# Optimization experiments

Hardware: AMD Instinct MI355X
Metric: run time of the kernel (lower is better)

Reference implementation:

```python
import jax, jax.numpy as jnp
import numpy as np

N, C, H, W, K = 8, 32, 512, 512, 6   # batch, embed dim, image HW, max components per image
MIN_PIX = 20
EPS = 1e-6
MARGIN = 0.5
L_INTER, L_INST, L_BG, L_SCENE = 0.4, 0.1, 0.2, 0.5


def _build_labels():
    # K disjoint 'subtitle line' rectangles per image; label 0 = background.
    # This is exactly what cv2.connectedComponents would return on the gt mask.
    labels = np.zeros((N, H, W), np.int32)
    for n in range(N):
        for k in range(K):
            r0 = 30 + k * 75
            c0 = 60 + (n % 3) * 20
            labels[n, r0:r0 + 40, c0:c0 + 300] = k + 1
    return labels


def setup_inputs() -> dict:
    key = jax.random.key(0)
    k1, k2 = jax.random.split(key)
    labels = _build_labels()
    gt = (labels > 0).astype(np.float32)[:, None]          # [N,1,H,W]
    color = jax.random.normal(k1, (N, C, H, W), jnp.float32)
    binary = jax.random.uniform(k2, (N, 1, H, W), jnp.float32)  # pred binary map
    return {"color": color, "gt": jnp.asarray(gt), "binary": binary,
            "comp_labels": jnp.asarray(labels)}


def _safe_norm(d2):
    # torch.norm = sqrt(sum sq); tiny floor avoids NaN grads at exactly 0
    return jnp.sqrt(jnp.maximum(d2, 1e-12))


def reference(color, gt, binary, comp_labels):
    f32 = color.dtype
    sub = (gt[:, 0] > 0.5).astype(f32)                                   # [N,H,W]
    text = (jax.lax.stop_gradient(binary)[:, 0] > 0.5).astype(f32)       # detached
    scene = text * (1.0 - sub)
    bg = (1.0 - sub) * (1.0 - scene)

    # one-hot component masks [N,K,H,W]
    comp = (comp_labels[:, None, :, :] ==
            jnp.arange(1, K + 1, dtype=comp_labels.dtype)[None, :, None, None]).astype(f32)
    cnt = comp.sum((2, 3))                                               # [N,K]

    # per-component first/second moments via batched segment-reduce
    S1 = jnp.einsum('nchw,nkhw->nkc', color, comp)                       # sum of feat
    fsq = (color * color).sum(1)                                         # [N,H,W]
    S2 = jnp.einsum('nhw,nkhw->nk', fsq, comp)                           # sum of |feat|^2
    m_inst = S1 / (cnt + EPS)[:, :, None]                                # [N,K,C]
    # sum over comp pixels of |f - m|^2, divided by (cnt+eps)
    intra_k = (S2 - 2.0 * (m_inst * S1).sum(-1)
               + cnt * (m_inst * m_inst).sum(-1)) / (cnt + EPS)

    sub_cnt = sub.sum((1, 2)); bg_cnt = bg.sum((1, 2)); scene_cnt = scene.sum((1, 2))
    m_sub = jnp.einsum('nchw,nhw->nc', color, sub) / (sub_cnt + EPS)[:, None]
    m_bg = jnp.einsum('nchw,nhw->nc', color, bg) / (bg_cnt + EPS)[:, None]
    m_scene = jnp.einsum('nchw,nhw->nc', color, scene) / (scene_cnt + EPS)[:, None]

    comp_big = cnt >= MIN_PIX                                            # [N,K]
    n_valid = comp_big.sum(1)                                            # [N]
    item_valid = (bg_cnt >= MIN_PIX) & (n_valid >= 1)
    cv = comp_big & item_valid[:, None]
    total = cv.sum()

    intra_sum = jnp.where(cv, intra_k, 0.0).sum()

    d_inst_bg = _safe_norm(((m_inst - m_bg[:, None, :]) ** 2).sum(-1))   # [N,K]
    inter_sum = jnp.where(cv, jax.nn.relu(MARGIN - d_inst_bg) ** 2, 0.0).sum()

    item_multi = item_valid & (n_valid > 1)
    d2_inst_sub = ((m_inst - m_sub[:, None, :]) ** 2).sum(-1)
    inst_sum = jnp.where(cv & item_multi[:, None], d2_inst_sub, 0.0).sum()
    inst_n = jnp.where(item_multi, n_valid, 0).sum()

    bg_cond = item_valid & (sub_cnt >= MIN_PIX)
    d_sub_bg = _safe_norm(((m_sub - m_bg) ** 2).sum(-1))
    subbg_sum = jnp.where(bg_cond, jax.nn.relu(MARGIN - d_sub_bg) ** 2, 0.0).sum()
    subbg_n = bg_cond.sum()

    sc_cond = item_valid & (scene_cnt >= MIN_PIX) & (sub_cnt >= MIN_PIX)
    d_sub_sc = _safe_norm(((m_sub - m_scene) ** 2).sum(-1))
    subsc_sum = jnp.where(sc_cond, jax.nn.relu(2.0 * MARGIN - d_sub_sc) ** 2, 0.0).sum()
    subsc_n = sc_cond.sum()

    def avg(s, n):
        return jnp.where(n > 0, s / jnp.maximum(n, 1).astype(f32), 0.0)

    loss = (avg(intra_sum, total)
            + L_INTER * avg(inter_sum, total)
            + L_INST * avg(inst_sum, inst_n)
            + L_BG * avg(subbg_sum, subbg_n)
            + L_SCENE * avg(subsc_sum, subsc_n))
    return jnp.where(total > 0, loss, jnp.zeros((), f32))
```

## Files before the change

kernel.cpp:

```cpp
#include <hip/hip_runtime.h>


#define NIMG   8
#define NCH    32
#define IMHW   (512 * 512)
#define STRIPE 1024
#define BPI    (IMHW / STRIPE)
#define WSN    304

__device__ __forceinline__ float redhalf(float x) {
    x += __shfl_xor(x, 1);
    x += __shfl_xor(x, 2);
    x += __shfl_xor(x, 4);
    x += __shfl_xor(x, 8);
    x += __shfl_xor(x, 16);
    return x;
}

__device__ __forceinline__ float red64(float x) {
    x += __shfl_xor(x, 1);
    x += __shfl_xor(x, 2);
    x += __shfl_xor(x, 4);
    x += __shfl_xor(x, 8);
    x += __shfl_xor(x, 16);
    x += __shfl_xor(x, 32);
    return x;
}

__device__ __forceinline__ void comp_pass(
    const float* __restrict__ colc, int pix0,
    const unsigned* __restrict__ codes, int l32, int c, int L2, float* lds)
{
    float aL = 0.f, s2 = 0.f;
#pragma unroll
    for (int j = 0; j < STRIPE; j += 128) {
        const int off = j + (l32 << 2);
        const float4 v4 = *reinterpret_cast<const float4*>(colc + pix0 + off);
        const unsigned cw = codes[off >> 2];
        const float vv[4] = {v4.x, v4.y, v4.z, v4.w};
#pragma unroll
        for (int e = 0; e < 4; ++e) {
            const int l = (int)((cw >> (8 * e + 2)) & 0x3Fu);
            const float mv = (l == L2) ? vv[e] : 0.f;
            aL += mv;
            s2 = fmaf(mv, mv, s2);
        }
    }
    aL = redhalf(aL); s2 = redhalf(s2);
    if (l32 == 0 && L2 >= 1 && L2 <= 6) {
        atomicAdd(&lds[96 + (L2 - 1) * 32 + c], aL);
        atomicAdd(&lds[297 + (L2 - 1)], s2);
    }
}

__global__ __launch_bounds__(256, 8) void scl_main(
    const float* __restrict__ color, const float* __restrict__ gt,
    const float* __restrict__ bin, const int* __restrict__ lab,
    float* __restrict__ ws)
{
    __shared__ float lds[WSN];
    __shared__ unsigned codes[STRIPE / 4];
    __shared__ int labmask;

    const int tid = threadIdx.x;
    for (int i = tid; i < WSN; i += 256) lds[i] = 0.f;
    if (tid == 0) labmask = 0;

    const int n    = blockIdx.x / BPI;
    const int pix0 = (blockIdx.x % BPI) * STRIPE;

    const float* gtn  = gt  + (size_t)n * IMHW;
    const float* binn = bin + (size_t)n * IMHW;
    const int*   labn = lab + (size_t)n * IMHW;
    const float* coln = color + (size_t)n * NCH * IMHW;

    const int off1 = tid << 2;
    {
        const int p = pix0 + off1;
        const float4 g4 = *reinterpret_cast<const float4*>(gtn + p);
        const float4 b4 = *reinterpret_cast<const float4*>(binn + p);
        const int4   l4 = *reinterpret_cast<const int4*>(labn + p);
        const float gg[4] = {g4.x, g4.y, g4.z, g4.w};
        const float bb[4] = {b4.x, b4.y, b4.z, b4.w};
        const int   ll[4] = {l4.x, l4.y, l4.z, l4.w};
        unsigned wrd = 0; int lm = 0;
        float c0 = 0.f, c1 = 0.f;
        float ck[6] = {0.f, 0.f, 0.f, 0.f, 0.f, 0.f};
#pragma unroll
        for (int e = 0; e < 4; ++e) {
            const bool sub  = gg[e] > 0.5f;
            const bool text = bb[e] > 0.5f;
            const int  r    = sub ? 0 : (text ? 1 : 2);
            const int  l    = ll[e];
            wrd |= (unsigned)((l << 2) | r) << (8 * e);
            lm  |= 1 << l;
            c0  += (r == 0) ? 1.f : 0.f;
            c1  += (r == 1) ? 1.f : 0.f;
#pragma unroll
            for (int kk = 0; kk < 6; ++kk)
                ck[kk] += (l == kk + 1) ? 1.f : 0.f;
        }
        codes[tid] = wrd;
        __syncthreads();

        c0 = red64(c0); c1 = red64(c1);
#pragma unroll
        for (int kk = 0; kk < 6; ++kk) ck[kk] = red64(ck[kk]);
        lm |= __shfl_xor(lm, 1);  lm |= __shfl_xor(lm, 2);
        lm |= __shfl_xor(lm, 4);  lm |= __shfl_xor(lm, 8);
        lm |= __shfl_xor(lm, 16); lm |= __shfl_xor(lm, 32);
        if ((tid & 63) == 0) {
            atomicAdd(&lds[288], c0);
            atomicAdd(&lds[289], c1);
#pragma unroll
            for (int kk = 0; kk < 6; ++kk) atomicAdd(&lds[291 + kk], ck[kk]);
            atomicOr(&labmask, lm);
        }
    }
    __syncthreads();

    const unsigned cmask = ((unsigned)labmask) & ~1u;
    const int Lc = cmask ? (__ffs(cmask) - 1) : 255;

    const int lane = tid & 63;
    const int wv   = tid >> 6;
    const int half = lane >> 5;
    const int l32  = lane & 31;

    for (int cpi = 0; cpi < 4; ++cpi) {
        const int cp = wv * 4 + cpi;
        const int c  = cp * 2 + half;
        const float* colc = coln + (size_t)c * IMHW;

        float vt = 0.f, s0 = 0.f, s1 = 0.f, aL = 0.f, s2 = 0.f;
#pragma unroll
        for (int j = 0; j < STRIPE; j += 128) {
            const int off = j + (l32 << 2);
            const float4 v4 = *reinterpret_cast<const float4*>(colc + pix0 + off);
            const unsigned cw = codes[off >> 2];
            const float vv[4] = {v4.x, v4.y, v4.z, v4.w};
#pragma unroll
            for (int e = 0; e < 4; ++e) {
                const float v = vv[e];
                const int r = (int)((cw >> (8 * e)) & 3u);
                const int l = (int)((cw >> (8 * e + 2)) & 0x3Fu);
                vt += v;
                s0 += (r == 0) ? v : 0.f;
                s1 += (r == 1) ? v : 0.f;
                const float mv = (l == Lc) ? v : 0.f;
                aL += mv;
                s2 = fmaf(mv, mv, s2);
            }
        }

        vt = redhalf(vt); s0 = redhalf(s0); s1 = redhalf(s1);
        aL = redhalf(aL); s2 = redhalf(s2);

        if (l32 == 0) {
            atomicAdd(&lds[ 0 + c], s0);
            atomicAdd(&lds[32 + c], s1);
            atomicAdd(&lds[64 + c], vt);
            if (Lc <= 6) {
                atomicAdd(&lds[96 + (Lc - 1) * 32 + c], aL);
                atomicAdd(&lds[297 + (Lc - 1)], s2);
            }
        }
    }

    unsigned extra = cmask ? (cmask & (cmask - 1)) : 0u;
    while (extra) {
        const int L2 = __ffs(extra) - 1; extra &= extra - 1;
        for (int cpi = 0; cpi < 4; ++cpi) {
            const int cp = wv * 4 + cpi;
            const int c  = cp * 2 + half;
            comp_pass(coln + (size_t)c * IMHW, pix0, codes, l32, c, L2, lds);
        }
    }
    __syncthreads();

    float* wsn = ws + (size_t)n * WSN;
    for (int i = tid; i < WSN; i += 256) {
        const float v = lds[i];
        if (v != 0.f) atomicAdd(&wsn[i], v);
    }
}

__global__ void scl_final(const float* __restrict__ ws, float* __restrict__ out)
{
    const int lane = threadIdx.x;
    const int n = lane / 6;
    const int k = lane - n * 6;
    const bool active = lane < 48;

    float t_cv = 0.f, t_intra = 0.f, t_inter = 0.f, t_inst = 0.f, t_instn = 0.f;
    float t_sbg = 0.f, t_sbgn = 0.f, t_ssc = 0.f, t_sscn = 0.f;

    if (active) {
        const float* w = ws + (size_t)n * WSN;
        const float cnt    = w[291 + k];
        const float s2     = w[297 + k];
        const float subc   = w[288];
        const float scenec = w[289];
        const float bgc    = 262144.f - subc - scenec;

        float nv = 0.f;
#pragma unroll
        for (int kk = 0; kk < 6; ++kk) nv += (w[291 + kk] >= 20.f) ? 1.f : 0.f;

        const bool comp_big   = cnt >= 20.f;
        const bool item_valid = (bgc >= 20.f) && (nv >= 1.f);
        const bool cv         = comp_big && item_valid;

        const float den  = cnt + 1e-6f;
        const float dsub = subc + 1e-6f;
        const float dbg  = bgc + 1e-6f;
        const float dsc  = scenec + 1e-6f;

        float dot_mS1 = 0.f, dot_mm = 0.f, d2bg = 0.f, d2sub = 0.f;
        for (int c = 0; c < 32; ++c) {
            const float S1 = w[96 + k * 32 + c];
            const float m  = S1 / den;
            dot_mS1 = fmaf(m, S1, dot_mS1);
            dot_mm  = fmaf(m, m, dot_mm);
            const float msub = w[c] / dsub;
            const float mbg  = (w[64 + c] - w[c] - w[32 + c]) / dbg;
            float d = m - mbg;  d2bg  = fmaf(d, d, d2bg);
            d = m - msub;       d2sub = fmaf(d, d, d2sub);
        }
        const float intra_k = (s2 - 2.f * dot_mS1 + cnt * dot_mm) / den;

        if (cv) {
            t_cv = 1.f;
            t_intra = intra_k;
            const float dd = sqrtf(fmaxf(d2bg, 1e-12f));
            const float r  = fmaxf(0.5f - dd, 0.f);
            t_inter = r * r;
        }
        const bool multi = item_valid && (nv > 1.f);
        if (cv && multi) t_inst = d2sub;

        if (k == 0) {
            if (multi) t_instn = nv;
            const bool bgcond = item_valid && (subc >= 20.f);
            const bool sccond = item_valid && (scenec >= 20.f) && (subc >= 20.f);
            float d2sb = 0.f, d2ss = 0.f;
            for (int c = 0; c < 32; ++c) {
                const float msub = w[c] / dsub;
                const float mbg  = (w[64 + c] - w[c] - w[32 + c]) / dbg;
                const float msc  = w[32 + c] / dsc;
                float a = msub - mbg; d2sb = fmaf(a, a, d2sb);
                float b = msub - msc; d2ss = fmaf(b, b, d2ss);
            }
            if (bgcond) {
                const float dd = sqrtf(fmaxf(d2sb, 1e-12f));
                const float r  = fmaxf(0.5f - dd, 0.f);
                t_sbg = r * r; t_sbgn = 1.f;
            }
            if (sccond) {
                const float dd = sqrtf(fmaxf(d2ss, 1e-12f));
                const float r  = fmaxf(1.0f - dd, 0.f);
                t_ssc = r * r; t_sscn = 1.f;
            }
        }
    }

#define RED64(x) { x += __shfl_xor(x, 1); x += __shfl_xor(x, 2); x += __shfl_xor(x, 4); \
                   x += __shfl_xor(x, 8); x += __shfl_xor(x, 16); x += __shfl_xor(x, 32); }
    RED64(t_cv) RED64(t_intra) RED64(t_inter) RED64(t_inst) RED64(t_instn)
    RED64(t_sbg) RED64(t_sbgn) RED64(t_ssc) RED64(t_sscn)
#undef RED64

    if (lane == 0) {
        const float total = t_cv;
        auto avg = [](float s, float nn) { return nn > 0.f ? s / fmaxf(nn, 1.f) : 0.f; };
        const float loss = avg(t_intra, total)
                         + 0.4f * avg(t_inter, total)
                         + 0.1f * avg(t_inst, t_instn)
                         + 0.2f * avg(t_sbg, t_sbgn)
                         + 0.5f * avg(t_ssc, t_sscn);
        out[0] = (total > 0.f) ? loss : 0.f;
    }
}

extern "C" void kernel_launch(void* const* d_in, const int* in_sizes, int n_in,
                              void* d_out, int out_size, void* d_ws, size_t ws_size,
                              hipStream_t stream)
{
    (void)in_sizes; (void)n_in; (void)out_size; (void)ws_size;
    const float* color = (const float*)d_in[0];
    const float* gt    = (const float*)d_in[1];
    const float* bin   = (const float*)d_in[2];
    const int*   lab   = (const int*)d_in[3];
    float* ws  = (float*)d_ws;
    float* out = (float*)d_out;

    hipMemsetAsync(ws, 0, (size_t)NIMG * WSN * sizeof(float), stream);
    hipLaunchKernelGGL(scl_main, dim3(NIMG * BPI), dim3(256), 0, stream,
                       color, gt, bin, lab, ws);
    hipLaunchKernelGGL(scl_final, dim3(1), dim3(64), 0, stream, ws, out);
}
```

Measured before the change: 404.8 us.

## Split mask coding into separate kernel and spread channels across four blocks

Moves the per-pixel mask/label coding into its own kernel that writes packed codes and per-chunk label masks to workspace. The color pass then launches four blocks per chunk, each handling 8 channels, which gives more parallelism and less serial work per block. Blocks now accumulate directly into global memory with atomics rather than through shared memory. The cost is an extra launch, a round trip for the codes through global memory, and more global atomic traffic.

```diff
diff --git a/kernel.cpp b/kernel.cpp
--- a/kernel.cpp
+++ b/kernel.cpp
@@ -4,184 +4,179 @@
 #define NIMG   8
 #define NCH    32
 #define IMHW   (512 * 512)
-#define STRIPE 1024
-#define BPI    (IMHW / STRIPE)
+#define CHUNK  1024
+#define CPI    (IMHW / CHUNK)
 #define WSN    304
+#define LC_OFF    12288
+#define CODES_OFF 16384
 
 __device__ __forceinline__ float redhalf(float x) {
-    x += __shfl_xor(x, 1);
-    x += __shfl_xor(x, 2);
-    x += __shfl_xor(x, 4);
-    x += __shfl_xor(x, 8);
-    x += __shfl_xor(x, 16);
+    x += __shfl_xor(x, 1);  x += __shfl_xor(x, 2);  x += __shfl_xor(x, 4);
+    x += __shfl_xor(x, 8);  x += __shfl_xor(x, 16);
     return x;
 }
-
 __device__ __forceinline__ float red64(float x) {
-    x += __shfl_xor(x, 1);
-    x += __shfl_xor(x, 2);
-    x += __shfl_xor(x, 4);
-    x += __shfl_xor(x, 8);
-    x += __shfl_xor(x, 16);
-    x += __shfl_xor(x, 32);
-    return x;
-}
-
-__device__ __forceinline__ void comp_pass(
-    const float* __restrict__ colc, int pix0,
-    const unsigned* __restrict__ codes, int l32, int c, int L2, float* lds)
+    x = redhalf(x); x += __shfl_xor(x, 32); return x;
+}
+
+__global__ __launch_bounds__(256) void scl_codes(
+    const float* __restrict__ gt, const float* __restrict__ bin,
+    const int* __restrict__ lab, float* __restrict__ ws,
+    unsigned char* __restrict__ lc, unsigned* __restrict__ codes)
 {
-    float aL = 0.f, s2 = 0.f;
-#pragma unroll
-    for (int j = 0; j < STRIPE; j += 128) {
-        const int off = j + (l32 << 2);
-        const float4 v4 = *reinterpret_cast<const float4*>(colc + pix0 + off);
-        const unsigned cw = codes[off >> 2];
-        const float vv[4] = {v4.x, v4.y, v4.z, v4.w};
-#pragma unroll
-        for (int e = 0; e < 4; ++e) {
-            const int l = (int)((cw >> (8 * e + 2)) & 0x3Fu);
-            const float mv = (l == L2) ? vv[e] : 0.f;
-            aL += mv;
-            s2 = fmaf(mv, mv, s2);
-        }
-    }
-    aL = redhalf(aL); s2 = redhalf(s2);
-    if (l32 == 0 && L2 >= 1 && L2 <= 6) {
-        atomicAdd(&lds[96 + (L2 - 1) * 32 + c], aL);
-        atomicAdd(&lds[297 + (L2 - 1)], s2);
-    }
-}
-
-__global__ __launch_bounds__(256, 8) void scl_main(
-    const float* __restrict__ color, const float* __restrict__ gt,
-    const float* __restrict__ bin, const int* __restrict__ lab,
+    __shared__ float ldsc[8];
+    __shared__ int labmask;
+    const int tid = threadIdx.x;
+    if (tid < 8) ldsc[tid] = 0.f;
+    if (tid == 0) labmask = 0;
+
+    const int n = blockIdx.x / CPI;
+    const int q = blockIdx.x % CPI;
+    const int base = n * IMHW + q * CHUNK;
+    const int p = base + (tid << 2);
+
+    const float4 g4 = *reinterpret_cast<const float4*>(gt + p);
+    const float4 b4 = *reinterpret_cast<const float4*>(bin + p);
+    const int4   l4 = *reinterpret_cast<const int4*>(lab + p);
+    const float gg[4] = {g4.x, g4.y, g4.z, g4.w};
+    const float bb[4] = {b4.x, b4.y, b4.z, b4.w};
+    const int   ll[4] = {l4.x, l4.y, l4.z, l4.w};
+
+    unsigned wrd = 0; int lm = 0;
+    float c0 = 0.f, c1 = 0.f;
+    float ck[6] = {0.f, 0.f, 0.f, 0.f, 0.f, 0.f};
+#pragma unroll
+    for (int e = 0; e < 4; ++e) {
+        const bool sub  = gg[e] > 0.5f;
+        const bool text = bb[e] > 0.5f;
+        const int  r    = sub ? 0 : (text ? 1 : 2);
+        unsigned   ul   = (unsigned)ll[e];
+        if (ul > 7u) ul = 7u;
+        wrd |= ((ul << 2) | (unsigned)r) << (8 * e);
+        lm  |= 1 << ul;
+        c0  += (r == 0) ? 1.f : 0.f;
+        c1  += (r == 1) ? 1.f : 0.f;
+#pragma unroll
+        for (int kk = 0; kk < 6; ++kk)
+            ck[kk] += (ul == (unsigned)(kk + 1)) ? 1.f : 0.f;
+    }
+    codes[(base >> 2) + tid] = wrd;
+
+    c0 = red64(c0); c1 = red64(c1);
+#pragma unroll
+    for (int kk = 0; kk < 6; ++kk) ck[kk] = red64(ck[kk]);
+    lm |= __shfl_xor(lm, 1);  lm |= __shfl_xor(lm, 2);  lm |= __shfl_xor(lm, 4);
+    lm |= __shfl_xor(lm, 8);  lm |= __shfl_xor(lm, 16); lm |= __shfl_xor(lm, 32);
+
+    __syncthreads();
+    if ((tid & 63) == 0) {
+        atomicAdd(&ldsc[0], c0);
+        atomicAdd(&ldsc[1], c1);
+#pragma unroll
+        for (int kk = 0; kk < 6; ++kk) atomicAdd(&ldsc[2 + kk], ck[kk]);
+        atomicOr(&labmask, lm);
+    }
+    __syncthreads();
+
+    float* wsn = ws + (size_t)n * WSN;
+    if (tid == 0) {
+        lc[n * CPI + q] = (unsigned char)((labmask >> 1) & 0x3F);
+        atomicAdd(&wsn[288], ldsc[0]);
+        atomicAdd(&wsn[289], ldsc[1]);
+    }
+    if (tid >= 2 && tid < 8) atomicAdd(&wsn[291 + (tid - 2)], ldsc[tid]);
+}
+
+__global__ __launch_bounds__(256) void scl_color(
+    const float* __restrict__ color, const float* __restrict__ ws_ro,
+    const unsigned char* __restrict__ lc, const unsigned* __restrict__ codes,
     float* __restrict__ ws)
 {
-    __shared__ float lds[WSN];
-    __shared__ unsigned codes[STRIPE / 4];
-    __shared__ int labmask;
-
-    const int tid = threadIdx.x;
-    for (int i = tid; i < WSN; i += 256) lds[i] = 0.f;
-    if (tid == 0) labmask = 0;
-
-    const int n    = blockIdx.x / BPI;
-    const int pix0 = (blockIdx.x % BPI) * STRIPE;
-
-    const float* gtn  = gt  + (size_t)n * IMHW;
-    const float* binn = bin + (size_t)n * IMHW;
-    const int*   labn = lab + (size_t)n * IMHW;
-    const float* coln = color + (size_t)n * NCH * IMHW;
-
-    const int off1 = tid << 2;
-    {
-        const int p = pix0 + off1;
-        const float4 g4 = *reinterpret_cast<const float4*>(gtn + p);
-        const float4 b4 = *reinterpret_cast<const float4*>(binn + p);
-        const int4   l4 = *reinterpret_cast<const int4*>(labn + p);
-        const float gg[4] = {g4.x, g4.y, g4.z, g4.w};
-        const float bb[4] = {b4.x, b4.y, b4.z, b4.w};
-        const int   ll[4] = {l4.x, l4.y, l4.z, l4.w};
-        unsigned wrd = 0; int lm = 0;
-        float c0 = 0.f, c1 = 0.f;
-        float ck[6] = {0.f, 0.f, 0.f, 0.f, 0.f, 0.f};
-#pragma unroll
-        for (int e = 0; e < 4; ++e) {
-            const bool sub  = gg[e] > 0.5f;
-            const bool text = bb[e] > 0.5f;
-            const int  r    = sub ? 0 : (text ? 1 : 2);
-            const int  l    = ll[e];
-            wrd |= (unsigned)((l << 2) | r) << (8 * e);
-            lm  |= 1 << l;
-            c0  += (r == 0) ? 1.f : 0.f;
-            c1  += (r == 1) ? 1.f : 0.f;
-#pragma unroll
-            for (int kk = 0; kk < 6; ++kk)
-                ck[kk] += (l == kk + 1) ? 1.f : 0.f;
-        }
-        codes[tid] = wrd;
-        __syncthreads();
-
-        c0 = red64(c0); c1 = red64(c1);
-#pragma unroll
-        for (int kk = 0; kk < 6; ++kk) ck[kk] = red64(ck[kk]);
-        lm |= __shfl_xor(lm, 1);  lm |= __shfl_xor(lm, 2);
-        lm |= __shfl_xor(lm, 4);  lm |= __shfl_xor(lm, 8);
-        lm |= __shfl_xor(lm, 16); lm |= __shfl_xor(lm, 32);
-        if ((tid & 63) == 0) {
-            atomicAdd(&lds[288], c0);
-            atomicAdd(&lds[289], c1);
-#pragma unroll
-            for (int kk = 0; kk < 6; ++kk) atomicAdd(&lds[291 + kk], ck[kk]);
-            atomicOr(&labmask, lm);
-        }
-    }
-    __syncthreads();
-
-    const unsigned cmask = ((unsigned)labmask) & ~1u;
-    const int Lc = cmask ? (__ffs(cmask) - 1) : 255;
-
+    __shared__ unsigned ldsC[CHUNK / 4];
+    (void)ws_ro;
+
+    const int bid = blockIdx.x;
+    const int g = bid & 3;
+    const int q = (bid >> 2) & (CPI - 1);
+    const int n = bid >> 10;
+
+    const int tid  = threadIdx.x;
     const int lane = tid & 63;
     const int wv   = tid >> 6;
     const int half = lane >> 5;
     const int l32  = lane & 31;
 
-    for (int cpi = 0; cpi < 4; ++cpi) {
-        const int cp = wv * 4 + cpi;
-        const int c  = cp * 2 + half;
-        const float* colc = coln + (size_t)c * IMHW;
-
-        float vt = 0.f, s0 = 0.f, s1 = 0.f, aL = 0.f, s2 = 0.f;
-#pragma unroll
-        for (int j = 0; j < STRIPE; j += 128) {
+    const int base = n * IMHW + q * CHUNK;
+    ldsC[tid] = codes[(base >> 2) + tid];
+
+    const unsigned mask6 = lc[n * CPI + q];
+    const int Lc = mask6 ? __ffs(mask6) : 255;
+
+    const int c = g * 8 + wv * 2 + half;
+    const float* colc = color + ((size_t)n * NCH + c) * IMHW + q * CHUNK;
+
+    __syncthreads();
+
+    float vt = 0.f, s0 = 0.f, s1 = 0.f, aL = 0.f, s2 = 0.f;
+#pragma unroll
+    for (int j = 0; j < CHUNK; j += 128) {
+        const int off = j + (l32 << 2);
+        const float4 v4 = *reinterpret_cast<const float4*>(colc + off);
+        const unsigned cw = ldsC[off >> 2];
+        const float vv[4] = {v4.x, v4.y, v4.z, v4.w};
+#pragma unroll
+        for (int e = 0; e < 4; ++e) {
+            const float v = vv[e];
+            const int r = (int)((cw >> (8 * e)) & 3u);
+            const int l = (int)((cw >> (8 * e + 2)) & 0x3Fu);
+            vt += v;
+            s0 += (r == 0) ? v : 0.f;
+            s1 += (r == 1) ? v : 0.f;
+            const float mv = (l == Lc) ? v : 0.f;
+            aL += mv;
+            s2 = fmaf(mv, mv, s2);
+        }
+    }
+
+    vt = redhalf(vt); s0 = redhalf(s0); s1 = redhalf(s1);
+    aL = redhalf(aL); s2 = redhalf(s2);
+    s2 += __shfl_xor(s2, 32);
+
+    float* wsn = ws + (size_t)n * WSN;
+    if (l32 == 0) {
+        atomicAdd(&wsn[ 0 + c], s0);
+        atomicAdd(&wsn[32 + c], s1);
+        atomicAdd(&wsn[64 + c], vt);
+        if (Lc >= 1 && Lc <= 6) {
+            atomicAdd(&wsn[96 + (Lc - 1) * 32 + c], aL);
+            if (lane == 0) atomicAdd(&wsn[297 + (Lc - 1)], s2);
+        }
+    }
+
+    unsigned extra = mask6 ? (mask6 & (mask6 - 1)) : 0u;
+    while (extra) {
+        const int L2 = __ffs(extra); extra &= extra - 1;
+        float aX = 0.f, sX = 0.f;
+#pragma unroll
+        for (int j = 0; j < CHUNK; j += 128) {
             const int off = j + (l32 << 2);
-            const float4 v4 = *reinterpret_cast<const float4*>(colc + pix0 + off);
-            const unsigned cw = codes[off >> 2];
+            const float4 v4 = *reinterpret_cast<const float4*>(colc + off);
+            const unsigned cw = ldsC[off >> 2];
             const float vv[4] = {v4.x, v4.y, v4.z, v4.w};
 #pragma unroll
             for (int e = 0; e < 4; ++e) {
-                const float v = vv[e];
-                const int r = (int)((cw >> (8 * e)) & 3u);
                 const int l = (int)((cw >> (8 * e + 2)) & 0x3Fu);
-                vt += v;
-                s0 += (r == 0) ? v : 0.f;
-                s1 += (r == 1) ? v : 0.f;
-                const float mv = (l == Lc) ? v : 0.f;
-                aL += mv;
-                s2 = fmaf(mv, mv, s2);
+                const float mv = (l == L2) ? vv[e] : 0.f;
+                aX += mv;
+                sX = fmaf(mv, mv, sX);
             }
         }
-
-        vt = redhalf(vt); s0 = redhalf(s0); s1 = redhalf(s1);
-        aL = redhalf(aL); s2 = redhalf(s2);
-
-        if (l32 == 0) {
-            atomicAdd(&lds[ 0 + c], s0);
-            atomicAdd(&lds[32 + c], s1);
-            atomicAdd(&lds[64 + c], vt);
-            if (Lc <= 6) {
-                atomicAdd(&lds[96 + (Lc - 1) * 32 + c], aL);
-                atomicAdd(&lds[297 + (Lc - 1)], s2);
-            }
-        }
-    }
-
-    unsigned extra = cmask ? (cmask & (cmask - 1)) : 0u;
-    while (extra) {
-        const int L2 = __ffs(extra) - 1; extra &= extra - 1;
-        for (int cpi = 0; cpi < 4; ++cpi) {
-            const int cp = wv * 4 + cpi;
-            const int c  = cp * 2 + half;
-            comp_pass(coln + (size_t)c * IMHW, pix0, codes, l32, c, L2, lds);
-        }
-    }
-    __syncthreads();
-
-    float* wsn = ws + (size_t)n * WSN;
-    for (int i = tid; i < WSN; i += 256) {
-        const float v = lds[i];
-        if (v != 0.f) atomicAdd(&wsn[i], v);
+        aX = redhalf(aX); sX = redhalf(sX);
+        sX += __shfl_xor(sX, 32);
+        if (l32 == 0 && L2 >= 1 && L2 <= 6) {
+            atomicAdd(&wsn[96 + (L2 - 1) * 32 + c], aX);
+            if (lane == 0) atomicAdd(&wsn[297 + (L2 - 1)], sX);
+        }
     }
 }
 
@@ -291,11 +286,15 @@
     const float* gt    = (const float*)d_in[1];
     const float* bin   = (const float*)d_in[2];
     const int*   lab   = (const int*)d_in[3];
-    float* ws  = (float*)d_ws;
+    float*          ws    = (float*)d_ws;
+    unsigned char*  lc    = (unsigned char*)d_ws + LC_OFF;
+    unsigned*       codes = (unsigned*)((char*)d_ws + CODES_OFF);
     float* out = (float*)d_out;
 
     hipMemsetAsync(ws, 0, (size_t)NIMG * WSN * sizeof(float), stream);
-    hipLaunchKernelGGL(scl_main, dim3(NIMG * BPI), dim3(256), 0, stream,
-                       color, gt, bin, lab, ws);
+    hipLaunchKernelGGL(scl_codes, dim3(NIMG * CPI), dim3(256), 0, stream,
+                       gt, bin, lab, ws, lc, codes);
+    hipLaunchKernelGGL(scl_color, dim3(NIMG * CPI * 4), dim3(256), 0, stream,
+                       color, ws, lc, codes, ws);
     hipLaunchKernelGGL(scl_final, dim3(1), dim3(64), 0, stream, ws, out);
 }
```

Result: slower. 449.8 us (+11.1%).

## Replace global atomics with per-block partial buffers and a separate reduce kernel

Applied to the files above, without the earlier changes.

Each block now handles a 2048-pixel stripe and writes its per-channel partial sums to a dedicated slot in a partial buffer instead of atomically adding into shared and then global memory. A new per-image reduce kernel sums those partials and scatters the component sums by each block's dominant label. Inner loads are batched four float4 at a time to raise memory-level parallelism. The change removes global atomic contention and halves the block count, at the cost of an extra kernel launch and fewer blocks to hide memory latency.

```diff
diff --git a/kernel.cpp b/kernel.cpp
--- a/kernel.cpp
+++ b/kernel.cpp
@@ -4,184 +4,260 @@
 #define NIMG   8
 #define NCH    32
 #define IMHW   (512 * 512)
-#define STRIPE 1024
+#define STRIPE 2048
 #define BPI    (IMHW / STRIPE)
 #define WSN    304
+#define PBS    144
+#define PB_OFF 16384
 
 __device__ __forceinline__ float redhalf(float x) {
-    x += __shfl_xor(x, 1);
-    x += __shfl_xor(x, 2);
-    x += __shfl_xor(x, 4);
-    x += __shfl_xor(x, 8);
-    x += __shfl_xor(x, 16);
+    x += __shfl_xor(x, 1);  x += __shfl_xor(x, 2);  x += __shfl_xor(x, 4);
+    x += __shfl_xor(x, 8);  x += __shfl_xor(x, 16);
     return x;
 }
-
 __device__ __forceinline__ float red64(float x) {
-    x += __shfl_xor(x, 1);
-    x += __shfl_xor(x, 2);
-    x += __shfl_xor(x, 4);
-    x += __shfl_xor(x, 8);
-    x += __shfl_xor(x, 16);
-    x += __shfl_xor(x, 32);
-    return x;
-}
-
-__device__ __forceinline__ void comp_pass(
-    const float* __restrict__ colc, int pix0,
-    const unsigned* __restrict__ codes, int l32, int c, int L2, float* lds)
-{
-    float aL = 0.f, s2 = 0.f;
-#pragma unroll
-    for (int j = 0; j < STRIPE; j += 128) {
-        const int off = j + (l32 << 2);
-        const float4 v4 = *reinterpret_cast<const float4*>(colc + pix0 + off);
-        const unsigned cw = codes[off >> 2];
-        const float vv[4] = {v4.x, v4.y, v4.z, v4.w};
-#pragma unroll
-        for (int e = 0; e < 4; ++e) {
-            const int l = (int)((cw >> (8 * e + 2)) & 0x3Fu);
-            const float mv = (l == L2) ? vv[e] : 0.f;
-            aL += mv;
-            s2 = fmaf(mv, mv, s2);
-        }
-    }
-    aL = redhalf(aL); s2 = redhalf(s2);
-    if (l32 == 0 && L2 >= 1 && L2 <= 6) {
-        atomicAdd(&lds[96 + (L2 - 1) * 32 + c], aL);
-        atomicAdd(&lds[297 + (L2 - 1)], s2);
-    }
-}
-
-__global__ __launch_bounds__(256, 8) void scl_main(
+    x = redhalf(x); x += __shfl_xor(x, 32); return x;
+}
+
+__global__ __launch_bounds__(256) void scl_main(
     const float* __restrict__ color, const float* __restrict__ gt,
     const float* __restrict__ bin, const int* __restrict__ lab,
-    float* __restrict__ ws)
+    float* __restrict__ stats, float* __restrict__ pb)
 {
-    __shared__ float lds[WSN];
     __shared__ unsigned codes[STRIPE / 4];
+    __shared__ float s2buf[16];
+    __shared__ float cnts[2];
+    __shared__ float cnt6[6];
     __shared__ int labmask;
 
     const int tid = threadIdx.x;
-    for (int i = tid; i < WSN; i += 256) lds[i] = 0.f;
+    if (tid < 2) cnts[tid] = 0.f;
+    if (tid < 6) cnt6[tid] = 0.f;
     if (tid == 0) labmask = 0;
 
     const int n    = blockIdx.x / BPI;
-    const int pix0 = (blockIdx.x % BPI) * STRIPE;
+    const int blk  = blockIdx.x % BPI;
+    const int pix0 = blk * STRIPE;
 
     const float* gtn  = gt  + (size_t)n * IMHW;
     const float* binn = bin + (size_t)n * IMHW;
     const int*   labn = lab + (size_t)n * IMHW;
     const float* coln = color + (size_t)n * NCH * IMHW;
 
-    const int off1 = tid << 2;
-    {
-        const int p = pix0 + off1;
+    float c0 = 0.f, c1 = 0.f;
+    float ck[6] = {0.f, 0.f, 0.f, 0.f, 0.f, 0.f};
+    int lm = 0;
+#pragma unroll
+    for (int jj = 0; jj < 2; ++jj) {
+        const int off = jj * 1024 + (tid << 2);
+        const int p   = pix0 + off;
         const float4 g4 = *reinterpret_cast<const float4*>(gtn + p);
         const float4 b4 = *reinterpret_cast<const float4*>(binn + p);
         const int4   l4 = *reinterpret_cast<const int4*>(labn + p);
         const float gg[4] = {g4.x, g4.y, g4.z, g4.w};
         const float bb[4] = {b4.x, b4.y, b4.z, b4.w};
         const int   ll[4] = {l4.x, l4.y, l4.z, l4.w};
-        unsigned wrd = 0; int lm = 0;
-        float c0 = 0.f, c1 = 0.f;
-        float ck[6] = {0.f, 0.f, 0.f, 0.f, 0.f, 0.f};
+        unsigned wrd = 0;
 #pragma unroll
         for (int e = 0; e < 4; ++e) {
             const bool sub  = gg[e] > 0.5f;
             const bool text = bb[e] > 0.5f;
             const int  r    = sub ? 0 : (text ? 1 : 2);
-            const int  l    = ll[e];
-            wrd |= (unsigned)((l << 2) | r) << (8 * e);
-            lm  |= 1 << l;
+            unsigned   ul   = (unsigned)ll[e];
+            if (ul > 7u) ul = 7u;
+            wrd |= ((ul << 2) | (unsigned)r) << (8 * e);
+            lm  |= 1 << ul;
             c0  += (r == 0) ? 1.f : 0.f;
             c1  += (r == 1) ? 1.f : 0.f;
 #pragma unroll
             for (int kk = 0; kk < 6; ++kk)
-                ck[kk] += (l == kk + 1) ? 1.f : 0.f;
-        }
-        codes[tid] = wrd;
-        __syncthreads();
-
-        c0 = red64(c0); c1 = red64(c1);
-#pragma unroll
-        for (int kk = 0; kk < 6; ++kk) ck[kk] = red64(ck[kk]);
-        lm |= __shfl_xor(lm, 1);  lm |= __shfl_xor(lm, 2);
-        lm |= __shfl_xor(lm, 4);  lm |= __shfl_xor(lm, 8);
-        lm |= __shfl_xor(lm, 16); lm |= __shfl_xor(lm, 32);
-        if ((tid & 63) == 0) {
-            atomicAdd(&lds[288], c0);
-            atomicAdd(&lds[289], c1);
-#pragma unroll
-            for (int kk = 0; kk < 6; ++kk) atomicAdd(&lds[291 + kk], ck[kk]);
-            atomicOr(&labmask, lm);
-        }
-    }
-    __syncthreads();
-
-    const unsigned cmask = ((unsigned)labmask) & ~1u;
-    const int Lc = cmask ? (__ffs(cmask) - 1) : 255;
+                ck[kk] += (ul == (unsigned)(kk + 1)) ? 1.f : 0.f;
+        }
+        codes[off >> 2] = wrd;
+    }
+    __syncthreads();
+
+    c0 = red64(c0); c1 = red64(c1);
+#pragma unroll
+    for (int kk = 0; kk < 6; ++kk) ck[kk] = red64(ck[kk]);
+    lm |= __shfl_xor(lm, 1);  lm |= __shfl_xor(lm, 2);  lm |= __shfl_xor(lm, 4);
+    lm |= __shfl_xor(lm, 8);  lm |= __shfl_xor(lm, 16); lm |= __shfl_xor(lm, 32);
+    if ((tid & 63) == 0) {
+        atomicAdd(&cnts[0], c0);
+        atomicAdd(&cnts[1], c1);
+#pragma unroll
+        for (int kk = 0; kk < 6; ++kk) atomicAdd(&cnt6[kk], ck[kk]);
+        atomicOr(&labmask, lm);
+    }
+    __syncthreads();
+
+    const unsigned cmask = (((unsigned)labmask) >> 1) & 0x3Fu;
+    const int Lc = cmask ? __ffs(cmask) : 255;
 
     const int lane = tid & 63;
     const int wv   = tid >> 6;
     const int half = lane >> 5;
     const int l32  = lane & 31;
+    float* pbb = pb + (size_t)blockIdx.x * PBS;
 
     for (int cpi = 0; cpi < 4; ++cpi) {
         const int cp = wv * 4 + cpi;
         const int c  = cp * 2 + half;
-        const float* colc = coln + (size_t)c * IMHW;
+        const float* colc = coln + (size_t)c * IMHW + pix0;
 
         float vt = 0.f, s0 = 0.f, s1 = 0.f, aL = 0.f, s2 = 0.f;
 #pragma unroll
-        for (int j = 0; j < STRIPE; j += 128) {
-            const int off = j + (l32 << 2);
-            const float4 v4 = *reinterpret_cast<const float4*>(colc + pix0 + off);
-            const unsigned cw = codes[off >> 2];
-            const float vv[4] = {v4.x, v4.y, v4.z, v4.w};
-#pragma unroll
-            for (int e = 0; e < 4; ++e) {
-                const float v = vv[e];
-                const int r = (int)((cw >> (8 * e)) & 3u);
-                const int l = (int)((cw >> (8 * e + 2)) & 0x3Fu);
-                vt += v;
-                s0 += (r == 0) ? v : 0.f;
-                s1 += (r == 1) ? v : 0.f;
-                const float mv = (l == Lc) ? v : 0.f;
-                aL += mv;
-                s2 = fmaf(mv, mv, s2);
-            }
+        for (int j0 = 0; j0 < STRIPE; j0 += 512) {
+            float4 a0, a1, a2, a3;
+            unsigned w0, w1, w2, w3;
+            {
+                const int o0 = j0 + 0 * 128 + (l32 << 2);
+                const int o1 = j0 + 1 * 128 + (l32 << 2);
+                const int o2 = j0 + 2 * 128 + (l32 << 2);
+                const int o3 = j0 + 3 * 128 + (l32 << 2);
+                a0 = *reinterpret_cast<const float4*>(colc + o0);
+                a1 = *reinterpret_cast<const float4*>(colc + o1);
+                a2 = *reinterpret_cast<const float4*>(colc + o2);
+                a3 = *reinterpret_cast<const float4*>(colc + o3);
+                w0 = codes[o0 >> 2]; w1 = codes[o1 >> 2];
+                w2 = codes[o2 >> 2]; w3 = codes[o3 >> 2];
+            }
+#define PROC(A, W) { \
+            const float vv[4] = {A.x, A.y, A.z, A.w}; \
+            _Pragma("unroll") \
+            for (int e = 0; e < 4; ++e) { \
+                const float v = vv[e]; \
+                const int r = (int)((W >> (8 * e)) & 3u); \
+                const int l = (int)((W >> (8 * e + 2)) & 0x3Fu); \
+                vt += v; \
+                s0 += (r == 0) ? v : 0.f; \
+                s1 += (r == 1) ? v : 0.f; \
+                const float mv = (l == Lc) ? v : 0.f; \
+                aL += mv; \
+                s2 = fmaf(mv, mv, s2); \
+            } }
+            PROC(a0, w0) PROC(a1, w1) PROC(a2, w2) PROC(a3, w3)
+#undef PROC
         }
 
         vt = redhalf(vt); s0 = redhalf(s0); s1 = redhalf(s1);
         aL = redhalf(aL); s2 = redhalf(s2);
+        s2 += __shfl_xor(s2, 32);
 
         if (l32 == 0) {
-            atomicAdd(&lds[ 0 + c], s0);
-            atomicAdd(&lds[32 + c], s1);
-            atomicAdd(&lds[64 + c], vt);
-            if (Lc <= 6) {
-                atomicAdd(&lds[96 + (Lc - 1) * 32 + c], aL);
-                atomicAdd(&lds[297 + (Lc - 1)], s2);
-            }
-        }
+            pbb[ 0 + c] = s0;
+            pbb[32 + c] = s1;
+            pbb[64 + c] = vt;
+            pbb[96 + c] = aL;
+            if (lane == 0) s2buf[cp] = s2;
+        }
+    }
+    __syncthreads();
+
+    if (tid == 0) {
+        float s2t = 0.f;
+#pragma unroll
+        for (int i = 0; i < 16; ++i) s2t += s2buf[i];
+        pbb[128] = s2t;
+        pbb[129] = cnts[0];
+        pbb[130] = cnts[1];
+        pbb[131] = (Lc >= 1 && Lc <= 6) ? cnt6[Lc - 1] : 0.f;
+        pbb[132] = (float)Lc;
     }
 
     unsigned extra = cmask ? (cmask & (cmask - 1)) : 0u;
+    if (extra && tid == 0) {
+        unsigned ex = extra;
+        while (ex) {
+            const int L2 = __ffs(ex); ex &= ex - 1;
+            atomicAdd(&stats[(size_t)n * WSN + 291 + (L2 - 1)], cnt6[L2 - 1]);
+        }
+    }
     while (extra) {
-        const int L2 = __ffs(extra) - 1; extra &= extra - 1;
+        const int L2 = __ffs(extra); extra &= extra - 1;
         for (int cpi = 0; cpi < 4; ++cpi) {
             const int cp = wv * 4 + cpi;
             const int c  = cp * 2 + half;
-            comp_pass(coln + (size_t)c * IMHW, pix0, codes, l32, c, L2, lds);
-        }
-    }
-    __syncthreads();
-
-    float* wsn = ws + (size_t)n * WSN;
-    for (int i = tid; i < WSN; i += 256) {
-        const float v = lds[i];
-        if (v != 0.f) atomicAdd(&wsn[i], v);
+            const float* colc = coln + (size_t)c * IMHW + pix0;
+            float aX = 0.f, sX = 0.f;
+            for (int j = 0; j < STRIPE; j += 128) {
+                const int off = j + (l32 << 2);
+                const float4 v4 = *reinterpret_cast<const float4*>(colc + off);
+                const unsigned cw = codes[off >> 2];
+                const float vv[4] = {v4.x, v4.y, v4.z, v4.w};
+#pragma unroll
+                for (int e = 0; e < 4; ++e) {
+                    const int l = (int)((cw >> (8 * e + 2)) & 0x3Fu);
+                    const float mv = (l == L2) ? vv[e] : 0.f;
+                    aX += mv;
+                    sX = fmaf(mv, mv, sX);
+                }
+            }
+            aX = redhalf(aX); sX = redhalf(sX);
+            sX += __shfl_xor(sX, 32);
+            if (l32 == 0) {
+                atomicAdd(&stats[(size_t)n * WSN + 96 + (L2 - 1) * 32 + c], aX);
+                if (lane == 0)
+                    atomicAdd(&stats[(size_t)n * WSN + 297 + (L2 - 1)], sX);
+            }
+        }
+    }
+}
+
+__global__ __launch_bounds__(256) void scl_reduce(
+    const float* __restrict__ pb, float* __restrict__ stats)
+{
+    __shared__ float comp[6][32];
+    __shared__ float comps2[6];
+    __shared__ float compcnt[6];
+
+    const int tid = threadIdx.x;
+    const int n   = blockIdx.x;
+    if (tid < 192) (&comp[0][0])[tid] = 0.f;
+    if (tid < 6) { comps2[tid] = 0.f; compcnt[tid] = 0.f; }
+    __syncthreads();
+
+    const float* base = pb + (size_t)n * BPI * PBS;
+    float* w = stats + (size_t)n * WSN;
+
+    if (tid < 96) {
+        const int c = tid & 31, row = tid >> 5;
+        float acc = 0.f;
+#pragma unroll 4
+        for (int q = 0; q < BPI; ++q) acc += base[q * PBS + row * 32 + c];
+        w[row * 32 + c] += acc;
+    } else if (tid < 128) {
+        const int c = tid - 96;
+#pragma unroll 4
+        for (int q = 0; q < BPI; ++q) {
+            const float a = base[q * PBS + 96 + c];
+            const int   L = (int)base[q * PBS + 132];
+            if (L >= 1 && L <= 6) atomicAdd(&comp[L - 1][c], a);
+        }
+    } else if (tid < 132) {
+        const int which = tid - 128;
+        float acc = 0.f;
+#pragma unroll 4
+        for (int q = 0; q < BPI; ++q) {
+            const float v = base[q * PBS + 128 + which];
+            if (which == 0 || which == 3) {
+                const int L = (int)base[q * PBS + 132];
+                if (L >= 1 && L <= 6)
+                    atomicAdd(which == 0 ? &comps2[L - 1] : &compcnt[L - 1], v);
+            } else acc += v;
+        }
+        if (which == 1) w[288] += acc;
+        if (which == 2) w[289] += acc;
+    }
+    __syncthreads();
+
+    if (tid < 32) {
+#pragma unroll
+        for (int kk = 0; kk < 6; ++kk) w[96 + kk * 32 + tid] += comp[kk][tid];
+    } else if (tid < 38) {
+        const int kk = tid - 32;
+        w[297 + kk] += comps2[kk];
+        w[291 + kk] += compcnt[kk];
     }
 }
 
@@ -291,11 +367,13 @@
     const float* gt    = (const float*)d_in[1];
     const float* bin   = (const float*)d_in[2];
     const int*   lab   = (const int*)d_in[3];
-    float* ws  = (float*)d_ws;
-    float* out = (float*)d_out;
-
-    hipMemsetAsync(ws, 0, (size_t)NIMG * WSN * sizeof(float), stream);
+    float* stats = (float*)d_ws;
+    float* pb    = (float*)((char*)d_ws + PB_OFF);
+    float* out   = (float*)d_out;
+
+    hipMemsetAsync(stats, 0, (size_t)NIMG * WSN * sizeof(float), stream);
     hipLaunchKernelGGL(scl_main, dim3(NIMG * BPI), dim3(256), 0, stream,
-                       color, gt, bin, lab, ws);
-    hipLaunchKernelGGL(scl_final, dim3(1), dim3(64), 0, stream, ws, out);
-}
+                       color, gt, bin, lab, stats, pb);
+    hipLaunchKernelGGL(scl_reduce, dim3(NIMG), dim3(256), 0, stream, pb, stats);
+    hipLaunchKernelGGL(scl_final, dim3(1), dim3(64), 0, stream, stats, out);
+}
```

Result: slower. 434.8 us (+7.4%).
